# Optimization experiments

Hardware: AMD Instinct MI355X
Metric: run time of the kernel (lower is better)

## Reference

```python
import jax, jax.numpy as jnp
import numpy as np

V = 25426          # tgt_vocab_size
D = 256            # d_model
H = 8              # heads
DH = 2048          # dim_head (d_ff passed positionally as d_head in source)
INNER = H * DH     # 16384
CLS = V            # cls token id (same value for t1 and t2 in source)
MASK_TOK = V + 2   # mask token id
VT = V + 3         # total embedding vocab


def _pos_encoding(n, d):
    pos = np.arange(n, dtype=np.float32)[:, None]
    div = np.exp(np.arange(0, d, 2, dtype=np.float32) * (-np.log(10000.0) / d))
    pe = np.zeros((n, d), dtype=np.float32)
    pe[:, 0::2] = np.sin(pos * div)
    pe[:, 1::2] = np.cos(pos * div)
    return jnp.asarray(pe)


def _layernorm(x, g, b, eps=1e-5):
    m = x.mean(-1, keepdims=True)
    v = ((x - m) ** 2).mean(-1, keepdims=True)
    return (x - m) / jnp.sqrt(v + eps) * g + b


def _cross_attn(x, ctx, pad_mask, Wq, Wk, Wv, Wo, bo):
    # x: [B,N,D], ctx: [B,M,Dc], pad_mask: [B,M] True = masked
    B, N, _ = x.shape
    M = ctx.shape[1]
    scale = DH ** -0.5
    q = (x @ Wq).reshape(B, N, H, DH)
    k = (ctx @ Wk).reshape(B, M, H, DH)
    v = (ctx @ Wv).reshape(B, M, H, DH)
    sim = jnp.einsum('bihd,bjhd->bhij', q, k) * scale  # [B,H,N,M]
    neg = -jnp.finfo(sim.dtype).max
    sim = jnp.where(pad_mask[:, None, None, :], neg, sim)
    attn = jax.nn.softmax(sim, axis=-1)
    out = jnp.einsum('bhij,bjhd->bihd', attn, v).reshape(B, N, INNER)
    return out @ Wo + bo


def _decoder(x, tgt_pad, src_mask, enc_output, p):
    a = _cross_attn(x, x, tgt_pad, p['Wq_s'], p['Wk_s'], p['Wv_s'], p['Wo_s'], p['bo_s'])
    x = _layernorm(x + a, p['g1'], p['be1'])
    a = _cross_attn(x, enc_output, src_mask, p['Wq_c'], p['Wk_c'], p['Wv_c'], p['Wo_c'], p['bo_c'])
    x = _layernorm(x + a, p['g2'], p['be2'])
    f = jax.nn.gelu(x @ p['W1'] + p['b1'], approximate=False) @ p['W2'] + p['b2']
    x = _layernorm(x + f, p['g3'], p['be3'])
    return x


def setup_inputs() -> dict:
    key = jax.random.key(0)
    ks = jax.random.split(key, 32)
    B, S, L = 2, 1024, 767
    d = {
        'src_input_id': jax.random.randint(ks[0], (B, S), 0, V),
        'tgt_input_id_t1': jax.random.randint(ks[1], (B, L), 0, V),
        'tgt_input_id_t2': jax.random.randint(ks[2], (B, L), 0, V),
        'original_lens': jax.random.randint(ks[3], (B,), 1, L),
        'enc_output': jax.random.normal(ks[4], (B, S, D), dtype=jnp.float32),
    }
    emb = jax.random.normal(ks[5], (VT, D), dtype=jnp.float32) * 0.02
    d['token_emb'] = emb.at[0].set(0.0)  # padding_idx=0
    s = 0.02
    d['Wq_s'] = jax.random.normal(ks[6], (D, INNER)) * s
    d['Wk_s'] = jax.random.normal(ks[7], (D, INNER)) * s
    d['Wv_s'] = jax.random.normal(ks[8], (D, INNER)) * s
    d['Wo_s'] = jax.random.normal(ks[9], (INNER, D)) * s
    d['bo_s'] = jnp.zeros((D,), jnp.float32)
    d['Wq_c'] = jax.random.normal(ks[10], (D, INNER)) * s
    d['Wk_c'] = jax.random.normal(ks[11], (D, INNER)) * s
    d['Wv_c'] = jax.random.normal(ks[12], (D, INNER)) * s
    d['Wo_c'] = jax.random.normal(ks[13], (INNER, D)) * s
    d['bo_c'] = jnp.zeros((D,), jnp.float32)
    d['W1'] = jax.random.normal(ks[14], (D, D)) * s  # Mlp hidden collapses to D (source bug)
    d['b1'] = jnp.zeros((D,), jnp.float32)
    d['W2'] = jax.random.normal(ks[15], (D, D)) * s
    d['b2'] = jnp.zeros((D,), jnp.float32)
    for i, n in enumerate(['g1', 'g2', 'g3']):
        d[n] = jnp.ones((D,), jnp.float32)
    for n in ['be1', 'be2', 'be3']:
        d[n] = jnp.zeros((D,), jnp.float32)
    d['Wfc'] = jax.random.normal(ks[16], (D, V)) * s
    d['bfc'] = jnp.zeros((V,), jnp.float32)
    return d


def reference(src_input_id, tgt_input_id_t1, tgt_input_id_t2, original_lens,
              enc_output, token_emb,
              Wq_s, Wk_s, Wv_s, Wo_s, bo_s,
              Wq_c, Wk_c, Wv_c, Wo_c, bo_c,
              W1, b1, W2, b2, g1, be1, g2, be2, g3, be3, Wfc, bfc):
    p = dict(Wq_s=Wq_s, Wk_s=Wk_s, Wv_s=Wv_s, Wo_s=Wo_s, bo_s=bo_s,
             Wq_c=Wq_c, Wk_c=Wk_c, Wv_c=Wv_c, Wo_c=Wo_c, bo_c=bo_c,
             W1=W1, b1=b1, W2=W2, b2=b2, g1=g1, be1=be1, g2=g2, be2=be2, g3=g3, be3=be3)
    B = tgt_input_id_t1.shape[0]
    cls = jnp.full((B, 1), CLS, dtype=tgt_input_id_t1.dtype)
    t1 = jnp.concatenate([cls, tgt_input_id_t1], axis=1)
    t2 = jnp.concatenate([cls, tgt_input_id_t2], axis=1)
    tgt = jnp.concatenate([t1, t2], axis=1)          # [B, T]
    tgt_pad = tgt == 0
    src_mask = src_input_id == 0
    # generate=True path: mask positions where id==mask_token or id==0
    tgt_mask = (tgt == MASK_TOK) | (tgt == 0)
    tgt_ids = jnp.where(tgt_mask, MASK_TOK, tgt)
    x = token_emb[tgt_ids]                            # [B, T, D]
    pe = _pos_encoding(x.shape[1], D)
    x = 2.0 * x + pe[None, :, :]                      # prepare_tokens: x + (x + pe), faithful to source
    x = _decoder(x, tgt_pad, src_mask, enc_output, p)
    logits = x @ Wfc + bfc
    return logits[:, 1:, :], x[:, 0, :]
```

## Files before the change

kernel.cpp:

```cpp
#include <hip/hip_runtime.h>
#include <hip/hip_bf16.h>
#include <float.h>
#include <math.h>

#define BB 2
#define SS 1024
#define LL 767
#define TT 1536
#define DD 256
#define HH 8
#define DHD 2048
#define INNER_ 16384
#define VV 25426
#define VPAD 25472
#define CLS_TOK 25426
#define MASK_TOKEN 25428
#define ROWS (BB*TT)
#define SROWS (BB*SS)

typedef __attribute__((ext_vector_type(8))) __bf16 bf16x8;
typedef __attribute__((ext_vector_type(4))) float f32x4;

__device__ __forceinline__ unsigned short f2bu(float f) {
    union { float f; unsigned u; } v; v.f = f;
    unsigned r = v.u + 0x7fff + ((v.u >> 16) & 1);
    return (unsigned short)(r >> 16);
}
__device__ __forceinline__ float bu2f(unsigned short u) {
    union { unsigned u; float f; } v; v.u = ((unsigned)u) << 16;
    return v.f;
}

__device__ __forceinline__ void gload16(const void* g, void* l) {
    __builtin_amdgcn_global_load_lds(
        (const __attribute__((address_space(1))) void*)g,
        (__attribute__((address_space(3))) void*)l, 16, 0, 0);
}


__global__ __launch_bounds__(256) void embed_kernel(
    const int* __restrict__ t1, const int* __restrict__ t2,
    const float* __restrict__ emb, float* __restrict__ x,
    unsigned short* __restrict__ xb, unsigned char* __restrict__ tgt_pad)
{
    int t = blockIdx.x, b = blockIdx.y, d = threadIdx.x;
    int raw;
    if (t == 0)            raw = CLS_TOK;
    else if (t <= LL)      raw = t1[b * LL + (t - 1)];
    else if (t == LL + 1)  raw = CLS_TOK;
    else                   raw = t2[b * LL + (t - LL - 2)];
    int id = (raw == 0 || raw == MASK_TOKEN) ? MASK_TOKEN : raw;
    int i = d >> 1;
    float ang = (float)t * expf(-0.03597789208f * (float)(2 * i));
    float pe = (d & 1) ? cosf(ang) : sinf(ang);
    float val = 2.f * emb[(long long)id * DD + d] + pe;
    long long idx = ((long long)(b * TT + t)) * DD + d;
    x[idx] = val;
    xb[idx] = f2bu(val);
    if (d == 0) tgt_pad[b * TT + t] = (raw == 0) ? 1 : 0;
}

__global__ __launch_bounds__(256) void masks_kernel(
    const int* __restrict__ src, unsigned char* __restrict__ m, int* __restrict__ rm)
{
    int i = blockIdx.x * 256 + threadIdx.x;
    if (i < SROWS) m[i] = (src[i] == 0) ? 1 : 0;
    if (i < ROWS) {
        int b = i / TT, t = i % TT;
        rm[i] = (t == 0) ? -1 : (b * (TT - 1) + t - 1);
    }
}

__global__ __launch_bounds__(256) void copycls_kernel(
    const float* __restrict__ x, float* __restrict__ out2)
{
    int b = blockIdx.x, d = threadIdx.x;
    out2[b * DD + d] = x[(long long)b * TT * DD + d];
}

__global__ __launch_bounds__(256) void conv_bf16v4(
    const float* __restrict__ in, unsigned short* __restrict__ out)
{
    size_t i = ((size_t)blockIdx.x * 256 + threadIdx.x) * 4;
    float4 v = *reinterpret_cast<const float4*>(in + i);
    ushort4 u;
    u.x = f2bu(v.x); u.y = f2bu(v.y); u.z = f2bu(v.z); u.w = f2bu(v.w);
    *reinterpret_cast<ushort4*>(out + i) = u;
}

__global__ __launch_bounds__(256) void convW6(
    const float* __restrict__ w0, const float* __restrict__ w1,
    const float* __restrict__ w2, const float* __restrict__ w3,
    const float* __restrict__ w4, const float* __restrict__ w5,
    unsigned short* __restrict__ dst)
{
    int seg = blockIdx.y;
    const float* s = seg == 0 ? w0 : seg == 1 ? w1 : seg == 2 ? w2 :
                     seg == 3 ? w3 : seg == 4 ? w4 : w5;
    size_t i = ((size_t)blockIdx.x * 256 + threadIdx.x) * 4;
    float4 v = *reinterpret_cast<const float4*>(s + i);
    ushort4 u;
    u.x = f2bu(v.x); u.y = f2bu(v.y); u.z = f2bu(v.z); u.w = f2bu(v.w);
    *reinterpret_cast<ushort4*>(dst + (size_t)seg * ((size_t)DD * INNER_) + i) = u;
}

__global__ __launch_bounds__(256) void transpose_conv(
    const float* __restrict__ in, unsigned short* __restrict__ out,
    int R, int Cin, int Nout)
{
    __shared__ float t[32][33];
    int k0 = blockIdx.x * 32, n0 = blockIdx.y * 32;
#pragma unroll
    for (int i = 0; i < 4; ++i) {
        int k = k0 + threadIdx.y + i * 8;
        int n = n0 + threadIdx.x;
        t[threadIdx.y + i * 8][threadIdx.x] = (n < Cin) ? in[(size_t)k * Cin + n] : 0.f;
    }
    __syncthreads();
#pragma unroll
    for (int i = 0; i < 4; ++i) {
        int n = n0 + threadIdx.y + i * 8;
        int k = k0 + threadIdx.x;
        out[(size_t)n * R + k] = f2bu(t[threadIdx.x][threadIdx.y + i * 8]);
    }
}

template<int STORE, int SPLITK>
__global__ __launch_bounds__(256) void gemm_bt(
    const unsigned short* __restrict__ A, int lda,
    const unsigned short* __restrict__ B, int ldb,
    void* __restrict__ Cv, int ldc,
    int M, int N, int K, float alpha, int zs,
    long long sAb, long long sAh, long long sBb, long long sBh,
    long long sCb, long long sCh,
    const float* __restrict__ bias, const int* __restrict__ rowmap)
{
    __shared__ unsigned short As[8192];
    __shared__ unsigned short Bs[8192];
    const int tid = threadIdx.x;
    const int w = tid >> 6, l = tid & 63;
    const int m0 = blockIdx.x * 128, n0 = blockIdx.y * 128;

    int kbeg = 0, kend = K;
    long long czoff = 0;
    if (SPLITK > 1) {
        constexpr int KSH = (SPLITK == 8) ? 3 : (SPLITK == 4) ? 2 : (SPLITK == 2) ? 1 : 0;
        int kidx = blockIdx.z & (SPLITK - 1);
        int zh = blockIdx.z >> KSH;
        int kc = K / SPLITK;
        kbeg = kidx * kc; kend = kbeg + kc;
        A += zh * sAh;
        B += zh * sBh;
        czoff = zh * sCh;
    } else {
        int zb = blockIdx.z >> zs;
        int zh = blockIdx.z - (zb << zs);
        A += zb * sAb + zh * sAh;
        B += zb * sBb + zh * sBh;
        czoff = zb * sCb + zh * sCh;
    }

    const int wr = (w >> 1) << 6, wc = (w & 1) << 6;
    const int lrow = l & 15, lk = l >> 4;

    const int sro = (w << 3) + (l >> 3);
    const int sko = (((l & 7) ^ (l >> 3)) << 3);
    const int ldst = (w << 10) + (l << 4);

    f32x4 acc[4][4];
#pragma unroll
    for (int mi = 0; mi < 4; ++mi)
#pragma unroll
        for (int ni = 0; ni < 4; ++ni)
            acc[mi][ni] = (f32x4){0.f, 0.f, 0.f, 0.f};

    for (int kt = kbeg; kt < kend; kt += 64) {
#pragma unroll
        for (int j = 0; j < 4; ++j)
            gload16(A + (size_t)(m0 + sro + j * 32) * lda + kt + sko,
                    (char*)As + (j << 12) + ldst);
#pragma unroll
        for (int j = 0; j < 4; ++j)
            gload16(B + (size_t)(n0 + sro + j * 32) * ldb + kt + sko,
                    (char*)Bs + (j << 12) + ldst);
        __syncthreads();

#pragma unroll
        for (int kk = 0; kk < 2; ++kk) {
            const int slot = (kk << 2) + lk;
            bf16x8 af[4], bfr[4];
#pragma unroll
            for (int mi = 0; mi < 4; ++mi) {
                int ra = wr + (mi << 4) + lrow;
                af[mi] = *reinterpret_cast<const bf16x8*>(
                    (const char*)As + (ra << 7) + ((slot ^ (ra & 7)) << 4));
            }
#pragma unroll
            for (int ni = 0; ni < 4; ++ni) {
                int rb = wc + (ni << 4) + lrow;
                bfr[ni] = *reinterpret_cast<const bf16x8*>(
                    (const char*)Bs + (rb << 7) + ((slot ^ (rb & 7)) << 4));
            }
#pragma unroll
            for (int mi = 0; mi < 4; ++mi)
#pragma unroll
                for (int ni = 0; ni < 4; ++ni)
                    acc[mi][ni] = __builtin_amdgcn_mfma_f32_16x16x32_bf16(
                        af[mi], bfr[ni], acc[mi][ni], 0, 0, 0);
        }
        __syncthreads();
    }

    if (STORE == 0) {
        unsigned short* C = (unsigned short*)Cv + czoff;
#pragma unroll
        for (int mi = 0; mi < 4; ++mi) {
            int r = m0 + wr + (mi << 4) + (lk << 2);
#pragma unroll
            for (int ni = 0; ni < 4; ++ni) {
                int c = n0 + wc + (ni << 4) + lrow;
#pragma unroll
                for (int q = 0; q < 4; ++q)
                    C[(size_t)(r + q) * ldc + c] = f2bu(acc[mi][ni][q] * alpha);
            }
        }
    } else if (STORE == 1) {
        unsigned short* C = (unsigned short*)Cv + czoff;
#pragma unroll
        for (int ni = 0; ni < 4; ++ni) {
            int c = n0 + wc + (ni << 4) + lrow;
#pragma unroll
            for (int mi = 0; mi < 4; ++mi) {
                int r = m0 + wr + (mi << 4) + (lk << 2);
                ushort4 u;
                u.x = f2bu(acc[mi][ni][0] * alpha);
                u.y = f2bu(acc[mi][ni][1] * alpha);
                u.z = f2bu(acc[mi][ni][2] * alpha);
                u.w = f2bu(acc[mi][ni][3] * alpha);
                *reinterpret_cast<ushort4*>(&C[(size_t)c * ldc + r]) = u;
            }
        }
    } else if (STORE == 2) {
        float* C = (float*)Cv;
#pragma unroll
        for (int mi = 0; mi < 4; ++mi) {
            int r = m0 + wr + (mi << 4) + (lk << 2);
#pragma unroll
            for (int q = 0; q < 4; ++q) {
                int rm = rowmap[r + q];
                if (rm < 0) continue;
#pragma unroll
                for (int ni = 0; ni < 4; ++ni) {
                    int c = n0 + wc + (ni << 4) + lrow;
                    if (c < N) C[(size_t)rm * ldc + c] = acc[mi][ni][q] * alpha + bias[c];
                }
            }
        }
    } else if (STORE == 3) {
        float* C = (float*)Cv + czoff;
#pragma unroll
        for (int mi = 0; mi < 4; ++mi) {
            int r = m0 + wr + (mi << 4) + (lk << 2);
#pragma unroll
            for (int ni = 0; ni < 4; ++ni) {
                int c = n0 + wc + (ni << 4) + lrow;
#pragma unroll
                for (int q = 0; q < 4; ++q)
                    atomicAdd(&C[(size_t)(r + q) * ldc + c], acc[mi][ni][q] * alpha);
            }
        }
    } else if (STORE == 4) {
        unsigned short* C = (unsigned short*)Cv + czoff;
#pragma unroll
        for (int mi = 0; mi < 4; ++mi) {
            int r = m0 + wr + (mi << 4) + (lk << 2);
#pragma unroll
            for (int ni = 0; ni < 4; ++ni) {
                int c = n0 + wc + (ni << 4) + lrow;
#pragma unroll
                for (int q = 0; q < 4; ++q) {
                    float v = acc[mi][ni][q] * alpha + bias[c];
                    v = 0.5f * v * (1.f + erff(v * 0.70710678118f));
                    C[(size_t)(r + q) * ldc + c] = f2bu(v);
                }
            }
        }
    } else {
        float* C = (float*)Cv + czoff;
#pragma unroll
        for (int mi = 0; mi < 4; ++mi) {
            int r = m0 + wr + (mi << 4) + (lk << 2);
#pragma unroll
            for (int ni = 0; ni < 4; ++ni) {
                int c = n0 + wc + (ni << 4) + lrow;
#pragma unroll
                for (int q = 0; q < 4; ++q)
                    C[(size_t)(r + q) * ldc + c] = acc[mi][ni][q] * alpha;
            }
        }
    }
}

template<int PPT>
__global__ __launch_bounds__(256) void softmax_bf16(
    unsigned short* __restrict__ S, const unsigned char* __restrict__ mask, int zs)
{
    __shared__ float red[4];
    const int z = blockIdx.y;
    const int RL = PPT * 512;
    ushort2* p = (ushort2*)(S + ((long long)z * TT + blockIdx.x) * RL);
    const uchar2* mk = (const uchar2*)(mask + (long long)(z >> zs) * RL);
    const int tid = threadIdx.x;

    float v[2 * PPT];
    float mx = -FLT_MAX;
#pragma unroll
    for (int c = 0; c < PPT; ++c) {
        int j = (c << 8) + tid;
        ushort2 u = p[j];
        uchar2 mm = mk[j];
        float s0 = mm.x ? -FLT_MAX : bu2f(u.x);
        float s1 = mm.y ? -FLT_MAX : bu2f(u.y);
        v[2 * c] = s0; v[2 * c + 1] = s1;
        mx = fmaxf(mx, fmaxf(s0, s1));
    }
#pragma unroll
    for (int off = 32; off > 0; off >>= 1) mx = fmaxf(mx, __shfl_down(mx, off));
    if ((tid & 63) == 0) red[tid >> 6] = mx;
    __syncthreads();
    mx = fmaxf(fmaxf(red[0], red[1]), fmaxf(red[2], red[3]));
    __syncthreads();

    float sum = 0.f;
#pragma unroll
    for (int c = 0; c < 2 * PPT; ++c) {
        float e = expf(v[c] - mx);
        v[c] = e;
        sum += e;
    }
#pragma unroll
    for (int off = 32; off > 0; off >>= 1) sum += __shfl_down(sum, off);
    if ((tid & 63) == 0) red[tid >> 6] = sum;
    __syncthreads();
    sum = red[0] + red[1] + red[2] + red[3];
    float inv = 1.f / sum;
#pragma unroll
    for (int c = 0; c < PPT; ++c) {
        int j = (c << 8) + tid;
        ushort2 u;
        u.x = f2bu(v[2 * c] * inv);
        u.y = f2bu(v[2 * c + 1] * inv);
        p[j] = u;
    }
}

__global__ __launch_bounds__(256) void ln_kernel(
    float* __restrict__ x, const float* __restrict__ a,
    const float* __restrict__ abias,
    const float* __restrict__ g, const float* __restrict__ be,
    unsigned short* __restrict__ xb)
{
    __shared__ float red[4];
    const long long r = blockIdx.x;
    const int d = threadIdx.x;
    const long long idx = r * DD + d;
    float v = x[idx] + a[idx];
    if (abias) v += abias[d];

    float s = v;
#pragma unroll
    for (int off = 32; off > 0; off >>= 1) s += __shfl_down(s, off);
    if ((d & 63) == 0) red[d >> 6] = s;
    __syncthreads();
    float mean = (red[0] + red[1] + red[2] + red[3]) * (1.f / DD);
    __syncthreads();

    float df = v - mean;
    float s2 = df * df;
#pragma unroll
    for (int off = 32; off > 0; off >>= 1) s2 += __shfl_down(s2, off);
    if ((d & 63) == 0) red[d >> 6] = s2;
    __syncthreads();
    float var = (red[0] + red[1] + red[2] + red[3]) * (1.f / DD);

    float o = df / sqrtf(var + 1e-5f) * g[d] + be[d];
    x[idx] = o;
    xb[idx] = f2bu(o);
}

extern "C" void kernel_launch(void* const* d_in, const int* in_sizes, int n_in,
                              void* d_out, int out_size, void* d_ws, size_t ws_size,
                              hipStream_t stream)
{
    const int*   src_ids = (const int*)d_in[0];
    const int*   t1      = (const int*)d_in[1];
    const int*   t2      = (const int*)d_in[2];
    const float* enc  = (const float*)d_in[4];
    const float* emb  = (const float*)d_in[5];
    const float* Wq_s = (const float*)d_in[6];
    const float* Wk_s = (const float*)d_in[7];
    const float* Wv_s = (const float*)d_in[8];
    const float* Wo_s = (const float*)d_in[9];
    const float* bo_s = (const float*)d_in[10];
    const float* Wq_c = (const float*)d_in[11];
    const float* Wk_c = (const float*)d_in[12];
    const float* Wv_c = (const float*)d_in[13];
    const float* Wo_c = (const float*)d_in[14];
    const float* bo_c = (const float*)d_in[15];
    const float* W1   = (const float*)d_in[16];
    const float* b1   = (const float*)d_in[17];
    const float* W2   = (const float*)d_in[18];
    const float* b2   = (const float*)d_in[19];
    const float* g1   = (const float*)d_in[20];
    const float* g2v  = (const float*)d_in[21];
    const float* g3   = (const float*)d_in[22];
    const float* be1  = (const float*)d_in[23];
    const float* be2  = (const float*)d_in[24];
    const float* be3  = (const float*)d_in[25];
    const float* Wfc  = (const float*)d_in[26];
    const float* bfc  = (const float*)d_in[27];

    char* p = (char*)d_ws;
    float* x    = (float*)p;           p += (size_t)ROWS * DD * 4;
    float* aout = (float*)p;           p += (size_t)ROWS * DD * 4;
    unsigned short* h1b  = (unsigned short*)p; p += (size_t)ROWS * DD * 2;
    unsigned short* xb   = (unsigned short*)p; p += (size_t)ROWS * DD * 2;
    unsigned short* encb = (unsigned short*)p; p += (size_t)SROWS * DD * 2;
    unsigned short* Wqb_s = (unsigned short*)p; p += (size_t)DD * INNER_ * 2;
    unsigned short* Wkb_s = (unsigned short*)p; p += (size_t)DD * INNER_ * 2;
    unsigned short* Wvb_s = (unsigned short*)p; p += (size_t)DD * INNER_ * 2;
    unsigned short* Wqb_c = (unsigned short*)p; p += (size_t)DD * INNER_ * 2;
    unsigned short* Wkb_c = (unsigned short*)p; p += (size_t)DD * INNER_ * 2;
    unsigned short* Wvb_c = (unsigned short*)p; p += (size_t)DD * INNER_ * 2;
    unsigned short* WoTs  = (unsigned short*)p; p += (size_t)DD * INNER_ * 2;
    unsigned short* WoTc  = (unsigned short*)p; p += (size_t)DD * INNER_ * 2;
    unsigned short* WfcT  = (unsigned short*)p; p += (size_t)VPAD * DD * 2;
    unsigned short* W1Tb  = (unsigned short*)p; p += (size_t)DD * DD * 2;
    unsigned short* W2Tb  = (unsigned short*)p; p += (size_t)DD * DD * 2;
    unsigned short* MtNb  = (unsigned short*)p; p += (size_t)4 * 524288 * 2;
    unsigned char* tgtpad = (unsigned char*)p; p += ROWS;
    unsigned char* srcpad = (unsigned char*)p; p += SROWS;
    p = (char*)(((size_t)p + 15) & ~(size_t)15);
    int* rowmap = (int*)p;             p += (size_t)ROWS * 4;

    unsigned short* Mtb_s = MtNb;
    unsigned short* Ntb_s = MtNb + 524288;
    unsigned short* Mtb_c = MtNb + 2 * 524288;
    unsigned short* Ntb_c = MtNb + 3 * 524288;

    unsigned short* ob = (unsigned short*)d_out;
    unsigned short* simS = ob;
    unsigned short* Pb   = ob + 37748736;
    unsigned short* YTb  = Pb + 6291456;
    float* MNacc = (float*)d_out;

    embed_kernel<<<dim3(TT, BB), 256, 0, stream>>>(t1, t2, emb, x, xb, tgtpad);
    masks_kernel<<<dim3(ROWS / 256), 256, 0, stream>>>(src_ids, srcpad, rowmap);
    conv_bf16v4<<<dim3((SROWS * DD) / 1024), 256, 0, stream>>>(enc, encb);

    dim3 tcb(32, 8);
    convW6<<<dim3((DD * INNER_) / 1024, 6), 256, 0, stream>>>(
        Wq_s, Wk_s, Wv_s, Wq_c, Wk_c, Wv_c, Wqb_s);
    transpose_conv<<<dim3(512, 8), tcb, 0, stream>>>(Wo_s, WoTs, INNER_, DD, DD);
    transpose_conv<<<dim3(512, 8), tcb, 0, stream>>>(Wo_c, WoTc, INNER_, DD, DD);
    transpose_conv<<<dim3(8, VPAD / 32), tcb, 0, stream>>>(Wfc, WfcT, DD, VV, VPAD);
    transpose_conv<<<dim3(8, 8), tcb, 0, stream>>>(W1, W1Tb, DD, DD, DD);
    transpose_conv<<<dim3(8, 8), tcb, 0, stream>>>(W2, W2Tb, DD, DD, DD);

    const float scale = 0.022097086912079608f;
    const long long Z0 = 0;

    hipMemsetAsync(MNacc, 0, (size_t)4 * 524288 * 4, stream);
    gemm_bt<3, 4><<<dim3(2, 2, 32), 256, 0, stream>>>(
        Wkb_s, INNER_, Wqb_s, INNER_, MNacc, 256, 256, 256, DHD, 1.f, 0,
        Z0, 2048, Z0, 2048, Z0, 65536, nullptr, nullptr);
    gemm_bt<3, 4><<<dim3(2, 2, 32), 256, 0, stream>>>(
        WoTs, INNER_, Wvb_s, INNER_, MNacc + 524288, 2048, 256, 256, DHD, 1.f, 0,
        Z0, 2048, Z0, 2048, Z0, 256, nullptr, nullptr);
    gemm_bt<3, 4><<<dim3(2, 2, 32), 256, 0, stream>>>(
        Wkb_c, INNER_, Wqb_c, INNER_, MNacc + 2 * 524288, 256, 256, 256, DHD, 1.f, 0,
        Z0, 2048, Z0, 2048, Z0, 65536, nullptr, nullptr);
    gemm_bt<3, 4><<<dim3(2, 2, 32), 256, 0, stream>>>(
        WoTc, INNER_, Wvb_c, INNER_, MNacc + 3 * 524288, 2048, 256, 256, DHD, 1.f, 0,
        Z0, 2048, Z0, 2048, Z0, 256, nullptr, nullptr);
    conv_bf16v4<<<dim3((4 * 524288) / 1024), 256, 0, stream>>>(MNacc, MtNb);

    hipMemsetAsync(aout, 0, (size_t)ROWS * DD * sizeof(float), stream);
    gemm_bt<0, 1><<<dim3(24, 2, 8), 256, 0, stream>>>(
        xb, DD, Mtb_s, DD, Pb, DD, ROWS, DD, DD, 1.f, 3,
        Z0, Z0, Z0, 65536, Z0, 786432, nullptr, nullptr);
    gemm_bt<1, 1><<<dim3(24, 2, 8), 256, 0, stream>>>(
        xb, DD, Ntb_s, 2048, YTb, ROWS, ROWS, DD, DD, 1.f, 3,
        Z0, Z0, Z0, 256, Z0, 786432, nullptr, nullptr);
    gemm_bt<0, 1><<<dim3(12, 12, 16), 256, 0, stream>>>(
        Pb, DD, xb, DD, simS, TT, TT, TT, DD, scale, 3,
        393216, 786432, 393216, Z0,
        18874368, 2359296, nullptr, nullptr);
    softmax_bf16<3><<<dim3(TT, 16), 256, 0, stream>>>(simS, tgtpad, 3);
    gemm_bt<3, 1><<<dim3(12, 2, 16), 256, 0, stream>>>(
        simS, TT, YTb, ROWS, aout, DD, TT, DD, TT, 1.f, 3,
        18874368, 2359296, 1536, 786432,
        393216, Z0, nullptr, nullptr);
    ln_kernel<<<dim3(ROWS), 256, 0, stream>>>(x, aout, bo_s, g1, be1, xb);

    hipMemsetAsync(aout, 0, (size_t)ROWS * DD * sizeof(float), stream);
    gemm_bt<0, 1><<<dim3(24, 2, 8), 256, 0, stream>>>(
        xb, DD, Mtb_c, DD, Pb, DD, ROWS, DD, DD, 1.f, 3,
        Z0, Z0, Z0, 65536, Z0, 786432, nullptr, nullptr);
    gemm_bt<1, 1><<<dim3(16, 2, 8), 256, 0, stream>>>(
        encb, DD, Ntb_c, 2048, YTb, SROWS, SROWS, DD, DD, 1.f, 3,
        Z0, Z0, Z0, 256, Z0, 524288, nullptr, nullptr);
    gemm_bt<0, 1><<<dim3(12, 8, 16), 256, 0, stream>>>(
        Pb, DD, encb, DD, simS, SS, TT, SS, DD, scale, 3,
        393216, 786432, 262144, Z0,
        12582912, 1572864, nullptr, nullptr);
    softmax_bf16<2><<<dim3(TT, 16), 256, 0, stream>>>(simS, srcpad, 3);
    gemm_bt<3, 1><<<dim3(12, 2, 16), 256, 0, stream>>>(
        simS, SS, YTb, SROWS, aout, DD, TT, DD, SS, 1.f, 3,
        12582912, 1572864, 1024, 524288,
        393216, Z0, nullptr, nullptr);
    ln_kernel<<<dim3(ROWS), 256, 0, stream>>>(x, aout, bo_c, g2v, be2, xb);

    gemm_bt<4, 1><<<dim3(24, 2, 1), 256, 0, stream>>>(
        xb, DD, W1Tb, DD, h1b, DD, ROWS, DD, DD, 1.f, 0,
        Z0, Z0, Z0, Z0, Z0, Z0, b1, nullptr);
    gemm_bt<5, 1><<<dim3(24, 2, 1), 256, 0, stream>>>(
        h1b, DD, W2Tb, DD, aout, DD, ROWS, DD, DD, 1.f, 0,
        Z0, Z0, Z0, Z0, Z0, Z0, nullptr, nullptr);
    ln_kernel<<<dim3(ROWS), 256, 0, stream>>>(x, aout, b2, g3, be3, xb);

    gemm_bt<2, 1><<<dim3(24, VPAD / 128, 1), 256, 0, stream>>>(
        xb, DD, WfcT, DD, d_out, VV, ROWS, VV, DD, 1.f, 0,
        Z0, Z0, Z0, Z0, Z0, Z0, bfc, rowmap);

    copycls_kernel<<<dim3(BB), 256, 0, stream>>>(
        x, (float*)d_out + (long long)BB * (TT - 1) * VV);
}
```

Baseline: 634.4 us.

## Fuse softmax into score GEMM epilogue with deferred row normalization

Drops the separate softmax kernel. The score GEMM epilogue now writes unnormalized exp(scale*s) as bf16 with pad masking and adds row sums into a workspace buffer. The PV GEMM then scales each row by the reciprocal sum before its atomic accumulation. This saves a full read and write pass over the large score matrices and one launch per attention. The exp is taken without subtracting the row max, so large scores could overflow, and the shared-memory and global atomics add contention.

```diff
diff --git a/kernel.cpp b/kernel.cpp
--- a/kernel.cpp
+++ b/kernel.cpp
@@ -285,72 +285,61 @@
                 }
             }
         }
+    } else if (STORE == 5) {
+        float* C = (float*)Cv + czoff;
+#pragma unroll
+        for (int mi = 0; mi < 4; ++mi) {
+            int r = m0 + wr + (mi << 4) + (lk << 2);
+#pragma unroll
+            for (int ni = 0; ni < 4; ++ni) {
+                int c = n0 + wc + (ni << 4) + lrow;
+#pragma unroll
+                for (int q = 0; q < 4; ++q)
+                    C[(size_t)(r + q) * ldc + c] = acc[mi][ni][q] * alpha;
+            }
+        }
+    } else if (STORE == 6) {
+        unsigned short* C = (unsigned short*)Cv + czoff;
+        const unsigned char* mrow =
+            (const unsigned char*)rowmap + (size_t)(blockIdx.z >> zs) * N;
+        float* rsum = (float*)bias;
+        float* sred = (float*)As;
+        if (tid < 128) sred[tid] = 0.f;
+        __syncthreads();
+#pragma unroll
+        for (int mi = 0; mi < 4; ++mi) {
+            int rl = wr + (mi << 4) + (lk << 2);
+#pragma unroll
+            for (int q = 0; q < 4; ++q) {
+                float rowacc = 0.f;
+#pragma unroll
+                for (int ni = 0; ni < 4; ++ni) {
+                    int c = n0 + wc + (ni << 4) + lrow;
+                    float e = mrow[c] ? 0.f : expf(acc[mi][ni][q] * alpha);
+                    C[(size_t)(m0 + rl + q) * ldc + c] = f2bu(e);
+                    rowacc += e;
+                }
+                atomicAdd(&sred[rl + q], rowacc);
+            }
+        }
+        __syncthreads();
+        if (tid < 128)
+            atomicAdd(&rsum[(size_t)blockIdx.z * M + m0 + tid], sred[tid]);
     } else {
         float* C = (float*)Cv + czoff;
 #pragma unroll
         for (int mi = 0; mi < 4; ++mi) {
             int r = m0 + wr + (mi << 4) + (lk << 2);
 #pragma unroll
-            for (int ni = 0; ni < 4; ++ni) {
-                int c = n0 + wc + (ni << 4) + lrow;
-#pragma unroll
-                for (int q = 0; q < 4; ++q)
-                    C[(size_t)(r + q) * ldc + c] = acc[mi][ni][q] * alpha;
-            }
-        }
-    }
-}
-
-template<int PPT>
-__global__ __launch_bounds__(256) void softmax_bf16(
-    unsigned short* __restrict__ S, const unsigned char* __restrict__ mask, int zs)
-{
-    __shared__ float red[4];
-    const int z = blockIdx.y;
-    const int RL = PPT * 512;
-    ushort2* p = (ushort2*)(S + ((long long)z * TT + blockIdx.x) * RL);
-    const uchar2* mk = (const uchar2*)(mask + (long long)(z >> zs) * RL);
-    const int tid = threadIdx.x;
-
-    float v[2 * PPT];
-    float mx = -FLT_MAX;
-#pragma unroll
-    for (int c = 0; c < PPT; ++c) {
-        int j = (c << 8) + tid;
-        ushort2 u = p[j];
-        uchar2 mm = mk[j];
-        float s0 = mm.x ? -FLT_MAX : bu2f(u.x);
-        float s1 = mm.y ? -FLT_MAX : bu2f(u.y);
-        v[2 * c] = s0; v[2 * c + 1] = s1;
-        mx = fmaxf(mx, fmaxf(s0, s1));
-    }
-#pragma unroll
-    for (int off = 32; off > 0; off >>= 1) mx = fmaxf(mx, __shfl_down(mx, off));
-    if ((tid & 63) == 0) red[tid >> 6] = mx;
-    __syncthreads();
-    mx = fmaxf(fmaxf(red[0], red[1]), fmaxf(red[2], red[3]));
-    __syncthreads();
-
-    float sum = 0.f;
-#pragma unroll
-    for (int c = 0; c < 2 * PPT; ++c) {
-        float e = expf(v[c] - mx);
-        v[c] = e;
-        sum += e;
-    }
-#pragma unroll
-    for (int off = 32; off > 0; off >>= 1) sum += __shfl_down(sum, off);
-    if ((tid & 63) == 0) red[tid >> 6] = sum;
-    __syncthreads();
-    sum = red[0] + red[1] + red[2] + red[3];
-    float inv = 1.f / sum;
-#pragma unroll
-    for (int c = 0; c < PPT; ++c) {
-        int j = (c << 8) + tid;
-        ushort2 u;
-        u.x = f2bu(v[2 * c] * inv);
-        u.y = f2bu(v[2 * c + 1] * inv);
-        p[j] = u;
+            for (int q = 0; q < 4; ++q) {
+                float rinv = 1.f / bias[(size_t)blockIdx.z * M + r + q];
+#pragma unroll
+                for (int ni = 0; ni < 4; ++ni) {
+                    int c = n0 + wc + (ni << 4) + lrow;
+                    atomicAdd(&C[(size_t)(r + q) * ldc + c], acc[mi][ni][q] * rinv);
+                }
+            }
+        }
     }
 }
 
@@ -423,6 +412,7 @@
     char* p = (char*)d_ws;
     float* x    = (float*)p;           p += (size_t)ROWS * DD * 4;
     float* aout = (float*)p;           p += (size_t)ROWS * DD * 4;
+    float* rsum = (float*)p;           p += (size_t)16 * TT * 4;
     unsigned short* h1b  = (unsigned short*)p; p += (size_t)ROWS * DD * 2;
     unsigned short* xb   = (unsigned short*)p; p += (size_t)ROWS * DD * 2;
     unsigned short* encb = (unsigned short*)p; p += (size_t)SROWS * DD * 2;
@@ -454,6 +444,8 @@
     unsigned short* YTb  = Pb + 6291456;
     float* MNacc = (float*)d_out;
 
+    const size_t accset = (size_t)ROWS * DD * 4 + (size_t)16 * TT * 4;
+
     embed_kernel<<<dim3(TT, BB), 256, 0, stream>>>(t1, t2, emb, x, xb, tgtpad);
     masks_kernel<<<dim3(ROWS / 256), 256, 0, stream>>>(src_ids, srcpad, rowmap);
     conv_bf16v4<<<dim3((SROWS * DD) / 1024), 256, 0, stream>>>(enc, encb);
@@ -485,40 +477,38 @@
         Z0, 2048, Z0, 2048, Z0, 256, nullptr, nullptr);
     conv_bf16v4<<<dim3((4 * 524288) / 1024), 256, 0, stream>>>(MNacc, MtNb);
 
-    hipMemsetAsync(aout, 0, (size_t)ROWS * DD * sizeof(float), stream);
+    hipMemsetAsync(aout, 0, accset, stream);
     gemm_bt<0, 1><<<dim3(24, 2, 8), 256, 0, stream>>>(
         xb, DD, Mtb_s, DD, Pb, DD, ROWS, DD, DD, 1.f, 3,
         Z0, Z0, Z0, 65536, Z0, 786432, nullptr, nullptr);
     gemm_bt<1, 1><<<dim3(24, 2, 8), 256, 0, stream>>>(
         xb, DD, Ntb_s, 2048, YTb, ROWS, ROWS, DD, DD, 1.f, 3,
         Z0, Z0, Z0, 256, Z0, 786432, nullptr, nullptr);
-    gemm_bt<0, 1><<<dim3(12, 12, 16), 256, 0, stream>>>(
+    gemm_bt<6, 1><<<dim3(12, 12, 16), 256, 0, stream>>>(
         Pb, DD, xb, DD, simS, TT, TT, TT, DD, scale, 3,
         393216, 786432, 393216, Z0,
-        18874368, 2359296, nullptr, nullptr);
-    softmax_bf16<3><<<dim3(TT, 16), 256, 0, stream>>>(simS, tgtpad, 3);
-    gemm_bt<3, 1><<<dim3(12, 2, 16), 256, 0, stream>>>(
+        18874368, 2359296, (const float*)rsum, (const int*)tgtpad);
+    gemm_bt<7, 1><<<dim3(12, 2, 16), 256, 0, stream>>>(
         simS, TT, YTb, ROWS, aout, DD, TT, DD, TT, 1.f, 3,
         18874368, 2359296, 1536, 786432,
-        393216, Z0, nullptr, nullptr);
+        393216, Z0, rsum, nullptr);
     ln_kernel<<<dim3(ROWS), 256, 0, stream>>>(x, aout, bo_s, g1, be1, xb);
 
-    hipMemsetAsync(aout, 0, (size_t)ROWS * DD * sizeof(float), stream);
+    hipMemsetAsync(aout, 0, accset, stream);
     gemm_bt<0, 1><<<dim3(24, 2, 8), 256, 0, stream>>>(
         xb, DD, Mtb_c, DD, Pb, DD, ROWS, DD, DD, 1.f, 3,
         Z0, Z0, Z0, 65536, Z0, 786432, nullptr, nullptr);
     gemm_bt<1, 1><<<dim3(16, 2, 8), 256, 0, stream>>>(
         encb, DD, Ntb_c, 2048, YTb, SROWS, SROWS, DD, DD, 1.f, 3,
         Z0, Z0, Z0, 256, Z0, 524288, nullptr, nullptr);
-    gemm_bt<0, 1><<<dim3(12, 8, 16), 256, 0, stream>>>(
+    gemm_bt<6, 1><<<dim3(12, 8, 16), 256, 0, stream>>>(
         Pb, DD, encb, DD, simS, SS, TT, SS, DD, scale, 3,
         393216, 786432, 262144, Z0,
-        12582912, 1572864, nullptr, nullptr);
-    softmax_bf16<2><<<dim3(TT, 16), 256, 0, stream>>>(simS, srcpad, 3);
-    gemm_bt<3, 1><<<dim3(12, 2, 16), 256, 0, stream>>>(
+        12582912, 1572864, (const float*)rsum, (const int*)srcpad);
+    gemm_bt<7, 1><<<dim3(12, 2, 16), 256, 0, stream>>>(
         simS, SS, YTb, SROWS, aout, DD, TT, DD, SS, 1.f, 3,
         12582912, 1572864, 1024, 524288,
-        393216, Z0, nullptr, nullptr);
+        393216, Z0, rsum, nullptr);
     ln_kernel<<<dim3(ROWS), 256, 0, stream>>>(x, aout, bo_c, g2v, be2, xb);
 
     gemm_bt<4, 1><<<dim3(24, 2, 1), 256, 0, stream>>>(
```

After: 656.3 us. 3.5% more time.
